# Kernel optimization log

Hardware: AMD Instinct MI355X
Metric: run time of the kernel (lower is better)

The kernel has to match this reference:

```python
import jax, jax.numpy as jnp
import numpy as np

N_NODES = 100000
N_EDGES = 3200000
IN_FEATS = 512
N_HIDDEN = 256
N_CLASSES = 16


def setup_inputs() -> dict:
    key = jax.random.key(0)
    k1, k2, k3, k4, k5, k6 = jax.random.split(key, 6)
    features = jax.random.normal(k1, (N_NODES, IN_FEATS), dtype=jnp.float32)
    edge_src = jax.random.randint(k2, (N_EDGES,), 0, N_NODES, dtype=jnp.int32)
    edge_dst = jax.random.randint(k3, (N_EDGES,), 0, N_NODES, dtype=jnp.int32)
    # Glorot-ish scaling for stability across 3 layers
    W1 = jax.random.normal(k4, (IN_FEATS, N_HIDDEN), dtype=jnp.float32) / np.sqrt(IN_FEATS)
    W2 = jax.random.normal(k5, (N_HIDDEN, N_HIDDEN), dtype=jnp.float32) / np.sqrt(N_HIDDEN)
    W3 = jax.random.normal(k6, (N_HIDDEN, N_CLASSES), dtype=jnp.float32) / np.sqrt(N_HIDDEN)
    return {"features": features, "edge_src": edge_src, "edge_dst": edge_dst,
            "W1": W1, "W2": W2, "W3": W3}


def graph_conv(feat, W, src, dst, n_nodes):
    # Dense projection (no bias), then copy_src + sum aggregation over edges.
    h = feat @ W                              # [N, out]
    msgs = h[src]                             # [E, out] gather from source nodes
    return jax.ops.segment_sum(msgs, dst, num_segments=n_nodes)  # [N, out]


def reference(features, edge_src, edge_dst, W1, W2, W3):
    h = graph_conv(features, W1, edge_src, edge_dst, N_NODES)
    h = graph_conv(h, W2, edge_src, edge_dst, N_NODES)
    h = graph_conv(h, W3, edge_src, edge_dst, N_NODES)
    return h
```

## Files before the change

### kernel.cpp

```cpp
#include <hip/hip_runtime.h>

#define NN 100000
#define NE 3200000
#define BS 512
#define NBUCK 196
#define EPB 12500
#define GEMM_BLKS 782

typedef short bf16x8 __attribute__((ext_vector_type(8)));
typedef float f32x4  __attribute__((ext_vector_type(4)));

__device__ inline unsigned rne_bf16(float x) {
    unsigned u = __float_as_uint(x);
    return (u + 0x7fffu + ((u >> 16) & 1u)) >> 16;
}
__device__ inline float bflo(unsigned u) { return __uint_as_float(u << 16); }
__device__ inline float bfhi(unsigned u) { return __uint_as_float(u & 0xffff0000u); }

__global__ __launch_bounds__(256) void l1_gemm_hist(const float* __restrict__ W2,
                                                    const float* __restrict__ W3,
                                                    float* __restrict__ M1,
                                                    const int* __restrict__ dst,
                                                    int* __restrict__ cntA) {
    __shared__ float As[16][260];
    __shared__ float Bs[256][16];
    __shared__ int hh[NBUCK];
    const int t = threadIdx.x;

    if (blockIdx.x < 16) {
        const int block_row = blockIdx.x * 16;
        for (int i = t; i < 1024; i += 256)
            ((float4*)&Bs[0][0])[i] = ((const float4*)W3)[i];
        for (int i = t; i < 1024; i += 256) {
            int idx = i << 2;
            int r = idx >> 8, c = idx & 255;
            int row = block_row + r;
            float4 v = ((const float4*)(W2 + (size_t)row * 256))[c >> 2];
            *(float4*)&As[r][c] = v;
        }
        __syncthreads();
        const int r = t >> 4, c = t & 15;
        float acc = 0.f;
#pragma unroll 8
        for (int k = 0; k < 256; ++k) acc += As[r][k] * Bs[k][c];
        M1[(size_t)(block_row + r) * 16 + c] = acc;
    } else {
        const int hb = blockIdx.x - 16;
        for (int i = t; i < NBUCK; i += 256) hh[i] = 0;
        __syncthreads();
        for (int e = hb * 256 + t; e < NE; e += 256 * 256)
            atomicAdd(&hh[dst[e] >> 9], 1);
        __syncthreads();
        for (int i = t; i < NBUCK; i += 256)
            if (hh[i]) atomicAdd(&cntA[i], hh[i]);
    }
}

__global__ __launch_bounds__(256) void gemm_n16t(const float* __restrict__ A,
                                                 const float* __restrict__ B,
                                                 unsigned short* __restrict__ Wt) {
    __shared__ float As[16][260];
    __shared__ float Bs[256][16];
    const int t = threadIdx.x;
    const int block_row = blockIdx.x * 16;

    for (int i = t; i < 1024; i += 256)
        ((float4*)&Bs[0][0])[i] = ((const float4*)B)[i];
    for (int i = t; i < 1024; i += 256) {
        int idx = i << 2;
        int r = idx >> 8, c = idx & 255;
        int row = block_row + r;
        float4 v = ((const float4*)(A + (size_t)row * 256))[c >> 2];
        *(float4*)&As[r][c] = v;
    }
    __syncthreads();
    const int r = t >> 4, c = t & 15;
    float acc = 0.f;
#pragma unroll 8
    for (int k = 0; k < 256; ++k) acc += As[r][k] * Bs[k][c];
    Wt[(size_t)c * 512 + block_row + r] = (unsigned short)rne_bf16(acc);
}

__global__ __launch_bounds__(512) void l3_binA_xwc(const int* __restrict__ src,
                                                   const int* __restrict__ dst,
                                                   const int* __restrict__ cntA,
                                                   int* __restrict__ cursorCnt,
                                                   unsigned* __restrict__ packed,
                                                   const float* __restrict__ X,
                                                   const unsigned short* __restrict__ WcT,
                                                   unsigned short* __restrict__ Yb) {
    __shared__ unsigned short As[128][72];
    __shared__ unsigned short Ws[16][520];
    __shared__ int sscan[256];
    __shared__ int baseL[NBUCK];
    __shared__ int hist[NBUCK];
    const int t = threadIdx.x;

    if (blockIdx.x < 256) {
        const int lo = blockIdx.x * EPB, hi = lo + EPB;
        int v = 0;
        if (t < 256) { v = (t < NBUCK) ? cntA[t] : 0; sscan[t] = v; }
        __syncthreads();
        for (int off = 1; off < 256; off <<= 1) {
            int u = 0;
            if (t < 256 && t >= off) u = sscan[t - off];
            __syncthreads();
            if (t < 256) sscan[t] += u;
            __syncthreads();
        }
        if (t < NBUCK) baseL[t] = sscan[t] - v;
        for (int i = t; i < NBUCK; i += 512) hist[i] = 0;
        __syncthreads();
        for (int i = lo + t; i < hi; i += 512)
            atomicAdd(&hist[dst[i] >> 9], 1);
        __syncthreads();
        for (int i = t; i < NBUCK; i += 512) {
            int c = hist[i];
            hist[i] = c ? baseL[i] + atomicAdd(&cursorCnt[i], c) : 0;
        }
        __syncthreads();
        for (int i = lo + t; i < hi; i += 512) {
            int d = dst[i];
            int pos = atomicAdd(&hist[d >> 9], 1);
            packed[pos] = ((unsigned)src[i] << 9) | (unsigned)(d & 511);
        }
    } else {
        const int brow = (blockIdx.x - 256) * 128;
        const int w = t >> 6, lane = t & 63;
        const int lrow = lane & 15, lk8 = (lane >> 4) * 8;

        for (int idx = t; idx < 1024; idx += 512) {
            int row = idx >> 6, ch = idx & 63;
            *(uint4*)&Ws[row][ch * 8] = ((const uint4*)(WcT + row * 512))[ch];
        }

        const int s_arow = t & 127, s_aq = t >> 7;
        const bool arow_ok = (brow + s_arow) < NN;
        const float* Ap0 = X + (size_t)(brow + s_arow) * 512 + s_aq * 16;

        f32x4 acc = {};

        for (int k0 = 0; k0 < 512; k0 += 64) {
            float4 f[4];
            if (arow_ok) {
                const float4* p = (const float4*)(Ap0 + k0);
#pragma unroll
                for (int i = 0; i < 4; ++i) f[i] = p[i];
            } else {
#pragma unroll
                for (int i = 0; i < 4; ++i) f[i] = make_float4(0.f, 0.f, 0.f, 0.f);
            }
            unsigned p8[8];
#pragma unroll
            for (int i = 0; i < 4; ++i) {
                p8[2 * i]     = rne_bf16(f[i].x) | (rne_bf16(f[i].y) << 16);
                p8[2 * i + 1] = rne_bf16(f[i].z) | (rne_bf16(f[i].w) << 16);
            }
            *(uint4*)&As[s_arow][s_aq * 16]     = make_uint4(p8[0], p8[1], p8[2], p8[3]);
            *(uint4*)&As[s_arow][s_aq * 16 + 8] = make_uint4(p8[4], p8[5], p8[6], p8[7]);
            __syncthreads();

#pragma unroll
            for (int ks = 0; ks < 2; ++ks) {
                bf16x8 af = *(const bf16x8*)&As[w * 16 + lrow][ks * 32 + lk8];
                bf16x8 bw = *(const bf16x8*)&Ws[lrow][k0 + ks * 32 + lk8];
                acc = __builtin_amdgcn_mfma_f32_16x16x32_bf16(af, bw, acc, 0, 0, 0);
            }
            __syncthreads();
        }

        const int col = lrow;
        const int rbase = brow + w * 16 + (lane >> 4) * 4;
#pragma unroll
        for (int r = 0; r < 4; ++r) {
            int row = rbase + r;
            if (row < NN)
                Yb[(size_t)row * 16 + col] = (unsigned short)rne_bf16(acc[r]);
        }
    }
}

__global__ __launch_bounds__(512) void binB(const unsigned* __restrict__ packed,
                                            const int* __restrict__ cntA,
                                            int* __restrict__ offs,
                                            int* __restrict__ srcs) {
    __shared__ int sscan[256];
    __shared__ int h[512];
    __shared__ int run[512];
    const int b = blockIdx.x, t = threadIdx.x;

    int v = 0;
    if (t < 256) { v = (t < NBUCK) ? cntA[t] : 0; sscan[t] = v; }
    __syncthreads();
    for (int off = 1; off < 256; off <<= 1) {
        int u = 0;
        if (t < 256 && t >= off) u = sscan[t - off];
        __syncthreads();
        if (t < 256) sscan[t] += u;
        __syncthreads();
    }
    const int hi = sscan[b];
    const int lo = hi - cntA[b];

    h[t] = 0;
    __syncthreads();
    for (int i = lo + t; i < hi; i += 512)
        atomicAdd(&h[packed[i] & 511], 1);
    __syncthreads();
    int mine = h[t];
    for (int off = 1; off < 512; off <<= 1) {
        int u = (t >= off) ? h[t - off] : 0;
        __syncthreads();
        h[t] += u;
        __syncthreads();
    }
    int gbase = lo + (h[t] - mine);
    int node = b * BS + t;
    if (node < NN) offs[node] = gbase;
    run[t] = gbase;
    __syncthreads();
    for (int i = lo + t; i < hi; i += 512) {
        unsigned v2 = packed[i];
        int pos = atomicAdd(&run[v2 & 511], 1);
        srcs[pos] = (int)(v2 >> 9);
    }
    if (b == NBUCK - 1 && t == 0) offs[NN] = NE;
}

template<bool OUT_F32>
__global__ __launch_bounds__(256) void agg16(const unsigned short* __restrict__ h,
                                             const int* __restrict__ offs,
                                             const int* __restrict__ srcs,
                                             void* __restrict__ outp) {
    int tid = blockIdx.x * 256 + threadIdx.x;
    int node = tid >> 2, f4 = tid & 3;
    if (node >= NN) return;
    int beg = offs[node], end = offs[node + 1];
    float a0 = 0, a1 = 0, a2 = 0, a3 = 0;
    float b0 = 0, b1 = 0, b2 = 0, b3 = 0;
    int j = beg;
    for (; j + 2 <= end; j += 2) {
        int s0 = srcs[j], s1 = srcs[j + 1];
        uint2 u = *(const uint2*)(h + (size_t)s0 * 16 + f4 * 4);
        uint2 v = *(const uint2*)(h + (size_t)s1 * 16 + f4 * 4);
        a0 += bflo(u.x); a1 += bfhi(u.x); a2 += bflo(u.y); a3 += bfhi(u.y);
        b0 += bflo(v.x); b1 += bfhi(v.x); b2 += bflo(v.y); b3 += bfhi(v.y);
    }
    if (j < end) {
        uint2 u = *(const uint2*)(h + (size_t)srcs[j] * 16 + f4 * 4);
        a0 += bflo(u.x); a1 += bfhi(u.x); a2 += bflo(u.y); a3 += bfhi(u.y);
    }
    float r0 = a0 + b0, r1 = a1 + b1, r2 = a2 + b2, r3 = a3 + b3;
    if (OUT_F32) {
        ((float4*)outp)[(size_t)node * 4 + f4] = make_float4(r0, r1, r2, r3);
    } else {
        uint2 r;
        r.x = rne_bf16(r0) | (rne_bf16(r1) << 16);
        r.y = rne_bf16(r2) | (rne_bf16(r3) << 16);
        ((uint2*)outp)[(size_t)node * 4 + f4] = r;
    }
}

extern "C" void kernel_launch(void* const* d_in, const int* in_sizes, int n_in,
                              void* d_out, int out_size, void* d_ws, size_t ws_size,
                              hipStream_t stream) {
    const float* X   = (const float*)d_in[0];
    const int*   src = (const int*)d_in[1];
    const int*   dst = (const int*)d_in[2];
    const float* W1  = (const float*)d_in[3];
    const float* W2  = (const float*)d_in[4];
    const float* W3  = (const float*)d_in[5];
    float* out = (float*)d_out;

    char* ws = (char*)d_ws;
    unsigned short* Yb = (unsigned short*)ws;   ws += (size_t)NN * 16 * 2;
    unsigned short* Gb = (unsigned short*)ws;   ws += (size_t)NN * 16 * 2;
    float* M1 = (float*)ws;                     ws += 256 * 16 * 4;
    unsigned short* WcT = (unsigned short*)ws;  ws += 16 * 512 * 2;
    unsigned* packed = (unsigned*)ws;           ws += (size_t)NE * 4;
    int* srcs       = (int*)ws;                 ws += (size_t)NE * 4;
    int* offs       = (int*)ws;                 ws += ((size_t)NN + 4) * 4;
    int* cntA       = (int*)ws;                 ws += 256 * 4;
    int* cursorCnt  = (int*)ws;                 ws += 256 * 4;

    hipMemsetAsync(cntA, 0, 512 * 4, stream);

    l1_gemm_hist<<<16 + 256, 256, 0, stream>>>(W2, W3, M1, dst, cntA);

    gemm_n16t<<<32, 256, 0, stream>>>(W1, M1, WcT);

    l3_binA_xwc<<<256 + GEMM_BLKS, 512, 0, stream>>>(src, dst, cntA, cursorCnt,
                                                     packed, X, WcT, Yb);

    binB<<<NBUCK, 512, 0, stream>>>(packed, cntA, offs, srcs);

    const int agg_blocks = (NN * 4 + 255) / 256;
    agg16<false><<<agg_blocks, 256, 0, stream>>>(Yb, offs, srcs, Gb);
    agg16<false><<<agg_blocks, 256, 0, stream>>>(Gb, offs, srcs, Yb);
    agg16<true ><<<agg_blocks, 256, 0, stream>>>(Yb, offs, srcs, out);
}
```

Measured before the change: 236.8 us.

## Split fused binning/GEMM kernel and make X·Wc GEMM register-only without LDS

New measurement: 293.6 us. +24.0%, slower.

```diff
diff --git a/kernel.cpp b/kernel.cpp
--- a/kernel.cpp
+++ b/kernel.cpp
@@ -5,7 +5,6 @@
 #define BS 512
 #define NBUCK 196
 #define EPB 12500
-#define GEMM_BLKS 782
 
 typedef short bf16x8 __attribute__((ext_vector_type(8)));
 typedef float f32x4  __attribute__((ext_vector_type(4)));
@@ -81,102 +80,84 @@
     Wt[(size_t)c * 512 + block_row + r] = (unsigned short)rne_bf16(acc);
 }
 
-__global__ __launch_bounds__(512) void l3_binA_xwc(const int* __restrict__ src,
-                                                   const int* __restrict__ dst,
-                                                   const int* __restrict__ cntA,
-                                                   int* __restrict__ cursorCnt,
-                                                   unsigned* __restrict__ packed,
-                                                   const float* __restrict__ X,
-                                                   const unsigned short* __restrict__ WcT,
-                                                   unsigned short* __restrict__ Yb) {
-    __shared__ unsigned short As[128][72];
-    __shared__ unsigned short Ws[16][520];
+__global__ __launch_bounds__(512) void binA(const int* __restrict__ src,
+                                            const int* __restrict__ dst,
+                                            const int* __restrict__ cntA,
+                                            int* __restrict__ cursorCnt,
+                                            unsigned* __restrict__ packed) {
     __shared__ int sscan[256];
     __shared__ int baseL[NBUCK];
     __shared__ int hist[NBUCK];
     const int t = threadIdx.x;
-
-    if (blockIdx.x < 256) {
-        const int lo = blockIdx.x * EPB, hi = lo + EPB;
-        int v = 0;
-        if (t < 256) { v = (t < NBUCK) ? cntA[t] : 0; sscan[t] = v; }
-        __syncthreads();
-        for (int off = 1; off < 256; off <<= 1) {
-            int u = 0;
-            if (t < 256 && t >= off) u = sscan[t - off];
-            __syncthreads();
-            if (t < 256) sscan[t] += u;
-            __syncthreads();
-        }
-        if (t < NBUCK) baseL[t] = sscan[t] - v;
-        for (int i = t; i < NBUCK; i += 512) hist[i] = 0;
-        __syncthreads();
-        for (int i = lo + t; i < hi; i += 512)
-            atomicAdd(&hist[dst[i] >> 9], 1);
-        __syncthreads();
-        for (int i = t; i < NBUCK; i += 512) {
-            int c = hist[i];
-            hist[i] = c ? baseL[i] + atomicAdd(&cursorCnt[i], c) : 0;
-        }
-        __syncthreads();
-        for (int i = lo + t; i < hi; i += 512) {
-            int d = dst[i];
-            int pos = atomicAdd(&hist[d >> 9], 1);
-            packed[pos] = ((unsigned)src[i] << 9) | (unsigned)(d & 511);
-        }
-    } else {
-        const int brow = (blockIdx.x - 256) * 128;
-        const int w = t >> 6, lane = t & 63;
-        const int lrow = lane & 15, lk8 = (lane >> 4) * 8;
-
-        for (int idx = t; idx < 1024; idx += 512) {
-            int row = idx >> 6, ch = idx & 63;
-            *(uint4*)&Ws[row][ch * 8] = ((const uint4*)(WcT + row * 512))[ch];
-        }
-
-        const int s_arow = t & 127, s_aq = t >> 7;
-        const bool arow_ok = (brow + s_arow) < NN;
-        const float* Ap0 = X + (size_t)(brow + s_arow) * 512 + s_aq * 16;
-
-        f32x4 acc = {};
-
-        for (int k0 = 0; k0 < 512; k0 += 64) {
-            float4 f[4];
-            if (arow_ok) {
-                const float4* p = (const float4*)(Ap0 + k0);
+    const int lo = blockIdx.x * EPB, hi = lo + EPB;
+
+    int v = 0;
+    if (t < 256) { v = (t < NBUCK) ? cntA[t] : 0; sscan[t] = v; }
+    __syncthreads();
+    for (int off = 1; off < 256; off <<= 1) {
+        int u = 0;
+        if (t < 256 && t >= off) u = sscan[t - off];
+        __syncthreads();
+        if (t < 256) sscan[t] += u;
+        __syncthreads();
+    }
+    if (t < NBUCK) baseL[t] = sscan[t] - v;
+    for (int i = t; i < NBUCK; i += 512) hist[i] = 0;
+    __syncthreads();
+    for (int i = lo + t; i < hi; i += 512)
+        atomicAdd(&hist[dst[i] >> 9], 1);
+    __syncthreads();
+    for (int i = t; i < NBUCK; i += 512) {
+        int c = hist[i];
+        hist[i] = c ? baseL[i] + atomicAdd(&cursorCnt[i], c) : 0;
+    }
+    __syncthreads();
+    for (int i = lo + t; i < hi; i += 512) {
+        int d = dst[i];
+        int pos = atomicAdd(&hist[d >> 9], 1);
+        packed[pos] = ((unsigned)src[i] << 9) | (unsigned)(d & 511);
+    }
+}
+
+__global__ __launch_bounds__(256) void gemm_xwc(const float* __restrict__ X,
+                                                const unsigned short* __restrict__ WcT,
+                                                unsigned short* __restrict__ Yb) {
+    const int t = threadIdx.x;
+    const int w = t >> 6, lane = t & 63;
+    const int lrow = lane & 15;
+    const int lk = (lane >> 4) * 8;
+    const int row_base = blockIdx.x * 64 + w * 16;
+
+    bf16x8 bfr[16];
+    const unsigned short* wp = WcT + lrow * 512 + lk;
 #pragma unroll
-                for (int i = 0; i < 4; ++i) f[i] = p[i];
-            } else {
+    for (int kk = 0; kk < 16; ++kk)
+        bfr[kk] = *(const bf16x8*)(wp + kk * 32);
+
+    const int arow = min(row_base + lrow, NN - 1);
+    const float* ap = X + (size_t)arow * 512 + lk;
+
+    f32x4 acc = {};
+#pragma unroll 4
+    for (int kk = 0; kk < 16; ++kk) {
+        const float4* p = (const float4*)(ap + kk * 32);
+        float4 a0 = p[0];
+        float4 a1 = p[1];
+        union { unsigned u[4]; bf16x8 v; } cvt;
+        cvt.u[0] = rne_bf16(a0.x) | (rne_bf16(a0.y) << 16);
+        cvt.u[1] = rne_bf16(a0.z) | (rne_bf16(a0.w) << 16);
+        cvt.u[2] = rne_bf16(a1.x) | (rne_bf16(a1.y) << 16);
+        cvt.u[3] = rne_bf16(a1.z) | (rne_bf16(a1.w) << 16);
+        acc = __builtin_amdgcn_mfma_f32_16x16x32_bf16(cvt.v, bfr[kk], acc, 0, 0, 0);
+    }
+
+    const int col = lane & 15;
+    const int rbase = row_base + (lane >> 4) * 4;
 #pragma unroll
-                for (int i = 0; i < 4; ++i) f[i] = make_float4(0.f, 0.f, 0.f, 0.f);
-            }
-            unsigned p8[8];
-#pragma unroll
-            for (int i = 0; i < 4; ++i) {
-                p8[2 * i]     = rne_bf16(f[i].x) | (rne_bf16(f[i].y) << 16);
-                p8[2 * i + 1] = rne_bf16(f[i].z) | (rne_bf16(f[i].w) << 16);
-            }
-            *(uint4*)&As[s_arow][s_aq * 16]     = make_uint4(p8[0], p8[1], p8[2], p8[3]);
-            *(uint4*)&As[s_arow][s_aq * 16 + 8] = make_uint4(p8[4], p8[5], p8[6], p8[7]);
-            __syncthreads();
-
-#pragma unroll
-            for (int ks = 0; ks < 2; ++ks) {
-                bf16x8 af = *(const bf16x8*)&As[w * 16 + lrow][ks * 32 + lk8];
-                bf16x8 bw = *(const bf16x8*)&Ws[lrow][k0 + ks * 32 + lk8];
-                acc = __builtin_amdgcn_mfma_f32_16x16x32_bf16(af, bw, acc, 0, 0, 0);
-            }
-            __syncthreads();
-        }
-
-        const int col = lrow;
-        const int rbase = brow + w * 16 + (lane >> 4) * 4;
-#pragma unroll
-        for (int r = 0; r < 4; ++r) {
-            int row = rbase + r;
-            if (row < NN)
-                Yb[(size_t)row * 16 + col] = (unsigned short)rne_bf16(acc[r]);
-        }
+    for (int r = 0; r < 4; ++r) {
+        int row = rbase + r;
+        if (row < NN)
+            Yb[(size_t)row * 16 + col] = (unsigned short)rne_bf16(acc[r]);
     }
 }
 
@@ -289,8 +270,9 @@
 
     gemm_n16t<<<32, 256, 0, stream>>>(W1, M1, WcT);
 
-    l3_binA_xwc<<<256 + GEMM_BLKS, 512, 0, stream>>>(src, dst, cntA, cursorCnt,
-                                                     packed, X, WcT, Yb);
+    binA<<<256, 512, 0, stream>>>(src, dst, cntA, cursorCnt, packed);
+
+    gemm_xwc<<<(NN + 63) / 64, 256, 0, stream>>>(X, WcT, Yb);
 
     binB<<<NBUCK, 512, 0, stream>>>(packed, cntA, offs, srcs);
 
```
